# Kernel tuning notes

Measured on AMD Instinct MI355X. Metric: run time of the kernel, lower is better.

Reference implementation:

```python
import jax, jax.numpy as jnp
import numpy as np
import math

B, S, D, H = 4, 2048, 512, 8
DK = D // H
EPS = 1e-6

def _xavier(key, shape):
    fan_in, fan_out = shape[1], shape[0]
    a = math.sqrt(6.0 / (fan_in + fan_out))
    return jax.random.uniform(key, shape, jnp.float32, -a, a)

def setup_inputs() -> dict:
    key = jax.random.key(0)
    ks = jax.random.split(key, 8)
    return {
        "x_q": jax.random.normal(ks[0], (B, S, D), jnp.float32),
        "x_k": jax.random.normal(ks[1], (B, S, D), jnp.float32),
        "Wq": _xavier(ks[2], (D, D)),
        "Wk": _xavier(ks[3], (D, D)),
        "Wv": _xavier(ks[4], (D, D)),
        "Wg": jnp.zeros((D, D), jnp.float32),      # gating weight init to 0
        "bg": jnp.ones((D,), jnp.float32),          # gating bias init to 1
        "Wo": _xavier(ks[5], (D, D)),
        "bo": jnp.zeros((D,), jnp.float32),
        "gamma": jnp.ones((D,), jnp.float32),
        "beta": jnp.zeros((D,), jnp.float32),
    }

def _ln(x, gamma, beta):
    mu = jnp.mean(x, axis=-1, keepdims=True)
    var = jnp.var(x, axis=-1, keepdims=True)
    return (x - mu) * jax.lax.rsqrt(var + EPS) * gamma + beta

def reference(x_q, x_k, Wq, Wk, Wv, Wg, bg, Wo, bo, gamma, beta):
    xq = _ln(x_q, gamma, beta)          # [B,S,D]
    xk = _ln(x_k, gamma, beta)
    q = xq @ Wq.T                        # nn.Linear: x @ W^T (no bias)
    k = xk @ Wk.T
    v = xk @ Wv.T
    q = q.reshape(B, S, H, DK)
    k = k.reshape(B, S, H, DK)
    v = v.reshape(B, S, H, DK)
    attn = jnp.einsum('bshd,bthd->bhst', q, k) / math.sqrt(DK)  # [B,H,S,S]
    attn = jax.nn.softmax(attn, axis=-1) * jax.nn.softmax(attn, axis=-2)
    out = jnp.einsum('bhst,bthd->bshd', attn, v).reshape(B, S, D)
    gate = jax.nn.sigmoid(xq @ Wg.T + bg)
    return (out * gate) @ Wo.T + bo
```

## Files before the change

kernel.cpp:

```cpp
#include <hip/hip_runtime.h>

#define BB 4
#define SS 2048
#define DD 512
#define HH 8
#define RR (BB * SS)
#define BH (BB * HH)

typedef unsigned short u16;
typedef unsigned int   u32;
typedef __attribute__((ext_vector_type(4))) float f32x4;
typedef __attribute__((ext_vector_type(8))) short bf16x8;

__device__ __forceinline__ float bf2f(u16 u) { return __uint_as_float(((u32)u) << 16); }
__device__ __forceinline__ u16 f2bf(float f) {
    u32 x = __float_as_uint(f);
    return (u16)((x + 0x7fffu + ((x >> 16) & 1u)) >> 16);
}
__device__ __forceinline__ bool is_bf16(const void* gamma) {
    return *(const u32*)gamma == 0x3F803F80u;
}
__device__ __forceinline__ float ldin(const void* p, size_t i, bool b16) {
    return b16 ? bf2f(((const u16*)p)[i]) : ((const float*)p)[i];
}
__device__ __forceinline__ float expc(float x) { return __expf(fminf(x, 60.f)); }
__device__ __forceinline__ float e2sum(float x) {
    return __builtin_amdgcn_exp2f(fminf(x * 1.44269504f, 86.5617f));
}
__device__ __forceinline__ float e2pv(float x) {
    return __builtin_amdgcn_exp2f(fminf(x * 2.88539008f, 86.5617f));
}

__global__ __launch_bounds__(256) void k_ln(
    const void* xq, const void* xk, const void* gamma, const void* beta,
    u16* __restrict__ lnq, u16* __restrict__ lnk, float* l_col)
{
    bool b16 = is_bf16(gamma);
    int row = blockIdx.x, tid = threadIdx.x;
    const void* x = blockIdx.y ? xk : xq;
    u16* o = blockIdx.y ? lnk : lnq;
    size_t base = (size_t)row * DD;

    if (blockIdx.y == 0 && row < 256) l_col[row * 256 + tid] = 0.f;

    float x0 = ldin(x, base + tid * 2, b16);
    float x1 = ldin(x, base + tid * 2 + 1, b16);
    float s = x0 + x1, ss = x0 * x0 + x1 * x1;
    for (int m = 1; m < 64; m <<= 1) { s += __shfl_xor(s, m); ss += __shfl_xor(ss, m); }
    __shared__ float ws4[4], wss4[4], mu_s, rs_s;
    int wv = tid >> 6;
    if ((tid & 63) == 0) { ws4[wv] = s; wss4[wv] = ss; }
    __syncthreads();
    if (tid == 0) {
        float S1 = ws4[0] + ws4[1] + ws4[2] + ws4[3];
        float S2 = wss4[0] + wss4[1] + wss4[2] + wss4[3];
        float mu = S1 / (float)DD;
        float var = S2 / (float)DD - mu * mu;
        mu_s = mu; rs_s = rsqrtf(fmaxf(var, 0.f) + 1e-6f);
    }
    __syncthreads();
    float mu = mu_s, rstd = rs_s;
    float g0 = ldin(gamma, tid * 2, b16), g1 = ldin(gamma, tid * 2 + 1, b16);
    float b0 = ldin(beta, tid * 2, b16),  b1 = ldin(beta, tid * 2 + 1, b16);
    o[base + tid * 2]     = f2bf((x0 - mu) * rstd * g0 + b0);
    o[base + tid * 2 + 1] = f2bf((x1 - mu) * rstd * g1 + b1);
}

__global__ __launch_bounds__(256) void k_proj4(
    const u16* __restrict__ lnq, const u16* __restrict__ lnk,
    const void* Wq, const void* Wk, const void* Wv, const void* Wg,
    const void* bg, const void* gamma,
    u16* __restrict__ qb, u16* __restrict__ kb,
    u16* __restrict__ vT, u16* __restrict__ gb)
{
    __shared__ __align__(16) u16 As[128][64];
    __shared__ __align__(16) u16 Bs[128][64];
    bool b16 = is_bf16(gamma);
    int which = blockIdx.z;
    const u16* A = (which <= 1) ? lnq : lnk;
    const void* W = (which == 0) ? Wq : (which == 1) ? Wg : (which == 2) ? Wk : Wv;
    u16* C = (which == 0) ? qb : (which == 1) ? gb : (which == 2) ? kb : vT;

    int tid = threadIdx.x;
    int lane = tid & 63, wave = tid >> 6;
    int r = lane & 15, q4 = lane >> 4;
    int m0 = blockIdx.y * 128, n0 = blockIdx.x * 128;
    int moff = (wave >> 1) * 64, noff = (wave & 1) * 64;
    const int K = DD, N = DD;

    f32x4 acc[4][4];
    for (int i = 0; i < 4; ++i)
        for (int j = 0; j < 4; ++j) acc[i][j] = (f32x4){0.f, 0.f, 0.f, 0.f};

    for (int k0 = 0; k0 < K; k0 += 64) {
        #pragma unroll
        for (int t = 0; t < 4; ++t) {
            int e = t * 2048 + tid * 8;
            int row = e >> 6, kk = e & 63;
            int ksw = kk ^ ((row & 7) * 8);
            *(uint4*)&As[row][ksw] = *(const uint4*)&A[(size_t)(m0 + row) * K + k0 + kk];
            if (b16) {
                *(uint4*)&Bs[row][ksw] =
                    *(const uint4*)&((const u16*)W)[(size_t)(n0 + row) * K + k0 + kk];
            } else {
                const float* wp = (const float*)W + (size_t)(n0 + row) * K + k0 + kk;
                float4 w0 = *(const float4*)wp;
                float4 w1 = *(const float4*)(wp + 4);
                ushort4 lo, hi;
                lo.x = f2bf(w0.x); lo.y = f2bf(w0.y); lo.z = f2bf(w0.z); lo.w = f2bf(w0.w);
                hi.x = f2bf(w1.x); hi.y = f2bf(w1.y); hi.z = f2bf(w1.z); hi.w = f2bf(w1.w);
                *(ushort4*)&Bs[row][ksw] = lo;
                *(ushort4*)&Bs[row][ksw + 4] = hi;
            }
        }
        __syncthreads();
        #pragma unroll
        for (int ksp = 0; ksp < 2; ++ksp) {
            int kb2 = ksp * 32 + q4 * 8;
            bf16x8 af[4], bfr[4];
            #pragma unroll
            for (int i = 0; i < 4; ++i) {
                int rowm = moff + i * 16 + r;
                af[i] = *(const bf16x8*)&As[rowm][kb2 ^ ((rowm & 7) * 8)];
                int rown = noff + i * 16 + r;
                bfr[i] = *(const bf16x8*)&Bs[rown][kb2 ^ ((rown & 7) * 8)];
            }
            #pragma unroll
            for (int i = 0; i < 4; ++i)
                #pragma unroll
                for (int j = 0; j < 4; ++j)
                    acc[i][j] = __builtin_amdgcn_mfma_f32_16x16x32_bf16(af[i], bfr[j], acc[i][j], 0, 0, 0);
        }
        __syncthreads();
    }

    if (which == 3) {
        int b = m0 >> 11;
        int sb = (m0 & 2047) + moff + q4 * 4;
        #pragma unroll
        for (int j = 0; j < 4; ++j) {
            int n = n0 + noff + j * 16 + r;
            int h = n >> 6, dkl = n & 63;
            size_t vbase = (((size_t)b * 8 + h) * 64 + dkl) * SS;
            #pragma unroll
            for (int i = 0; i < 4; ++i) {
                ushort4 wv;
                wv.x = f2bf(acc[i][j][0]); wv.y = f2bf(acc[i][j][1]);
                wv.z = f2bf(acc[i][j][2]); wv.w = f2bf(acc[i][j][3]);
                *(ushort4*)&C[vbase + sb + i * 16] = wv;
            }
        }
    } else {
        #pragma unroll
        for (int j = 0; j < 4; ++j) {
            int col = n0 + noff + j * 16 + r;
            float bj = (which == 1) ? ldin(bg, col, b16) : 0.f;
            #pragma unroll
            for (int i = 0; i < 4; ++i) {
                int rowb = m0 + moff + i * 16 + q4 * 4;
                #pragma unroll
                for (int g = 0; g < 4; ++g) {
                    float v = acc[i][j][g];
                    if (which == 1) v = 1.f / (1.f + expc(-(v + bj)));
                    else if (which == 0) v *= 0.125f;
                    C[(size_t)(rowb + g) * N + col] = f2bf(v);
                }
            }
        }
    }
}

__global__ __launch_bounds__(256) void k_sum(
    const u16* __restrict__ qm, const u16* __restrict__ km,
    float* __restrict__ l_row, float* __restrict__ l_col)
{
    __shared__ __align__(16) u16 Qs[64][64];
    __shared__ __align__(16) u16 Ks[128][64];
    __shared__ float colS[SS];
    int tid = threadIdx.x, lane = tid & 63, wave = tid >> 6;
    int r = lane & 15, q4 = lane >> 4;
    int s0 = blockIdx.x * 64;
    int bh = blockIdx.y, b = bh >> 3, h = bh & 7;
    size_t hb = (size_t)b * SS * DD + (size_t)h * 64;

    #pragma unroll
    for (int t = 0; t < 2; ++t) {
        int e = t * 2048 + tid * 8;
        int row = e >> 6, kk = e & 63;
        *(uint4*)&Qs[row][kk ^ ((row & 7) * 8)] = *(const uint4*)&qm[hb + (size_t)(s0 + row) * DD + kk];
    }
    for (int i = tid; i < SS; i += 256) colS[i] = 0.f;
    __syncthreads();

    int moff = wave * 16;
    bf16x8 aq[2];
    #pragma unroll
    for (int ksp = 0; ksp < 2; ++ksp) {
        int rowm = moff + r;
        aq[ksp] = *(const bf16x8*)&Qs[rowm][(ksp * 32 + q4 * 8) ^ ((rowm & 7) * 8)];
    }

    float rs[4] = {};
    for (int t0 = 0; t0 < SS; t0 += 128) {
        #pragma unroll
        for (int t = 0; t < 4; ++t) {
            int e = t * 2048 + tid * 8;
            int row = e >> 6, kk = e & 63;
            *(uint4*)&Ks[row][kk ^ ((row & 7) * 8)] = *(const uint4*)&km[hb + (size_t)(t0 + row) * DD + kk];
        }
        __syncthreads();

        f32x4 acc[8];
        for (int j = 0; j < 8; ++j) acc[j] = (f32x4){0.f, 0.f, 0.f, 0.f};
        #pragma unroll
        for (int ksp = 0; ksp < 2; ++ksp) {
            int kb2 = ksp * 32 + q4 * 8;
            bf16x8 bk[8];
            #pragma unroll
            for (int j = 0; j < 8; ++j) {
                int n = j * 16 + r;
                bk[j] = *(const bf16x8*)&Ks[n][kb2 ^ ((n & 7) * 8)];
            }
            #pragma unroll
            for (int j = 0; j < 8; ++j)
                acc[j] = __builtin_amdgcn_mfma_f32_16x16x32_bf16(aq[ksp], bk[j], acc[j], 0, 0, 0);
        }

        #pragma unroll
        for (int j = 0; j < 8; ++j) {
            float e0 = e2sum(acc[j][0]);
            float e1 = e2sum(acc[j][1]);
            float e2 = e2sum(acc[j][2]);
            float e3 = e2sum(acc[j][3]);
            rs[0] += e0; rs[1] += e1; rs[2] += e2; rs[3] += e3;
            float v = (e0 + e1) + (e2 + e3);
            v += __shfl_xor(v, 16); v += __shfl_xor(v, 32);
            if (q4 == 0) atomicAdd(&colS[t0 + j * 16 + r], v);
        }
        __syncthreads();
    }
    #pragma unroll
    for (int g = 0; g < 4; ++g) {
        float v = rs[g];
        v += __shfl_xor(v, 1); v += __shfl_xor(v, 2);
        v += __shfl_xor(v, 4); v += __shfl_xor(v, 8);
        if (r == 0) l_row[(size_t)bh * SS + s0 + moff + q4 * 4 + g] = v;
    }
    for (int i = tid; i < SS; i += 256)
        atomicAdd(&l_col[(size_t)bh * SS + i], colS[i]);
}

__global__ void k_rcp(const float* __restrict__ l_row, float* __restrict__ inv_r, int n)
{
    int i = blockIdx.x * blockDim.x + threadIdx.x;
    if (i < n) inv_r[i] = 1.f / fmaxf(l_row[i], 1e-30f);
}

__global__ __launch_bounds__(256) void k_vscale(
    u16* __restrict__ vT, const float* __restrict__ l_col)
{
    int row = blockIdx.x;
    int bh = row >> 6;
    int t = threadIdx.x * 8;
    size_t base = (size_t)row * SS + t;
    const float* lc = &l_col[(size_t)bh * SS + t];
    bf16x8 v = *(const bf16x8*)&vT[base];
    float4 c0 = *(const float4*)lc;
    float4 c1 = *(const float4*)(lc + 4);
    float s[8] = {1.f / fmaxf(c0.x, 1e-30f), 1.f / fmaxf(c0.y, 1e-30f),
                  1.f / fmaxf(c0.z, 1e-30f), 1.f / fmaxf(c0.w, 1e-30f),
                  1.f / fmaxf(c1.x, 1e-30f), 1.f / fmaxf(c1.y, 1e-30f),
                  1.f / fmaxf(c1.z, 1e-30f), 1.f / fmaxf(c1.w, 1e-30f)};
    bf16x8 o;
    #pragma unroll
    for (int e = 0; e < 8; ++e)
        o[e] = (short)f2bf(bf2f((u16)v[e]) * s[e]);
    *(bf16x8*)&vT[base] = o;
}

__global__ __launch_bounds__(256) void k_pv(
    const u16* __restrict__ qm, const u16* __restrict__ km, const u16* __restrict__ vT,
    const float* __restrict__ inv_r,
    const u16* __restrict__ gate, u16* __restrict__ og)
{
    __shared__ __align__(16) u16 Ep[64][128];
    __shared__ __align__(16) u16 KV[8192];
    int tid = threadIdx.x, lane = tid & 63, wave = tid >> 6;
    int r = lane & 15, q4 = lane >> 4;
    int s0 = blockIdx.x * 64;
    int bh = blockIdx.y, b = bh >> 3, h = bh & 7;
    size_t hb = (size_t)b * SS * DD + (size_t)h * 64;
    int moff = wave * 16;

    #pragma unroll
    for (int t = 0; t < 2; ++t) {
        int e = t * 2048 + tid * 8;
        int row = e >> 6, kk = e & 63;
        *(uint4*)&Ep[row][kk ^ ((row & 7) * 8)] = *(const uint4*)&qm[hb + (size_t)(s0 + row) * DD + kk];
    }
    __syncthreads();
    bf16x8 aq[2];
    #pragma unroll
    for (int ksp = 0; ksp < 2; ++ksp) {
        int rowm = moff + r;
        aq[ksp] = *(const bf16x8*)&Ep[rowm][(ksp * 32 + q4 * 8) ^ ((rowm & 7) * 8)];
    }
    __syncthreads();

    f32x4 acco[4];
    for (int j = 0; j < 4; ++j) acco[j] = (f32x4){0.f, 0.f, 0.f, 0.f};

    int sl = moff + r, swz = (sl & 7) * 8;

    for (int t0 = 0; t0 < SS; t0 += 128) {
        #pragma unroll
        for (int t = 0; t < 4; ++t) {
            int e = t * 2048 + tid * 8;
            int row = e >> 6, kk = e & 63;
            *(uint4*)&KV[row * 64 + (kk ^ ((row & 7) * 8))] =
                *(const uint4*)&km[hb + (size_t)(t0 + row) * DD + kk];
        }
        __syncthreads();

        f32x4 accs[8];
        #pragma unroll
        for (int m = 0; m < 8; ++m) accs[m] = (f32x4){0.f, 0.f, 0.f, 0.f};
        #pragma unroll
        for (int ksp = 0; ksp < 2; ++ksp) {
            int kb2 = ksp * 32 + q4 * 8;
            bf16x8 ak[8];
            #pragma unroll
            for (int m = 0; m < 8; ++m) {
                int n = m * 16 + r;
                ak[m] = *(const bf16x8*)&KV[n * 64 + (kb2 ^ ((n & 7) * 8))];
            }
            #pragma unroll
            for (int m = 0; m < 8; ++m)
                accs[m] = __builtin_amdgcn_mfma_f32_16x16x32_bf16(ak[m], aq[ksp], accs[m], 0, 0, 0);
        }
        __syncthreads();

        #pragma unroll
        for (int c = 0; c < 4; ++c) {
            int e = c * 256 + tid;
            int row = e >> 4, tc = (e & 15) * 8;
            *(uint4*)&KV[row * 128 + (tc ^ ((row & 7) * 8))] =
                *(const uint4*)&vT[((size_t)bh * 64 + row) * SS + t0 + tc];
        }
        #pragma unroll
        for (int m = 0; m < 8; ++m) {
            float p0 = e2pv(accs[m][0]);
            float p1 = e2pv(accs[m][1]);
            float p2 = e2pv(accs[m][2]);
            float p3 = e2pv(accs[m][3]);
            u32 w0, w1;
            asm("v_cvt_pk_bf16_f32 %0, %1, %2" : "=v"(w0) : "v"(p0), "v"(p1));
            asm("v_cvt_pk_bf16_f32 %0, %1, %2" : "=v"(w1) : "v"(p2), "v"(p3));
            uint2 pr; pr.x = w0; pr.y = w1;
            *(uint2*)&Ep[sl][(m * 16 + q4 * 4) ^ swz] = pr;
        }
        __syncthreads();

        #pragma unroll
        for (int ksp = 0; ksp < 4; ++ksp) {
            int kb2 = ksp * 32 + q4 * 8;
            bf16x8 ap = *(const bf16x8*)&Ep[sl][kb2 ^ swz];
            bf16x8 bv[4];
            #pragma unroll
            for (int j = 0; j < 4; ++j) {
                int n = j * 16 + r;
                bv[j] = *(const bf16x8*)&KV[n * 128 + (kb2 ^ ((n & 7) * 8))];
            }
            #pragma unroll
            for (int j = 0; j < 4; ++j)
                acco[j] = __builtin_amdgcn_mfma_f32_16x16x32_bf16(ap, bv[j], acco[j], 0, 0, 0);
        }
        __syncthreads();
    }

    #pragma unroll
    for (int g = 0; g < 4; ++g) {
        int srow = s0 + moff + q4 * 4 + g;
        float ir = inv_r[(size_t)bh * SS + srow];
        size_t ob = (size_t)b * SS * DD + (size_t)srow * DD + (size_t)h * 64;
        #pragma unroll
        for (int j = 0; j < 4; ++j) {
            int dk = j * 16 + r;
            og[ob + dk] = f2bf(acco[j][g] * ir * bf2f(gate[ob + dk]));
        }
    }
}

__global__ __launch_bounds__(256) void k_gemm_out(
    const u16* __restrict__ A, const void* W, const void* gamma,
    float* __restrict__ Cf, const void* bias)
{
    __shared__ __align__(16) u16 As[128][64];
    __shared__ __align__(16) u16 Bs[128][64];
    bool b16 = is_bf16(gamma);
    int tid = threadIdx.x;
    int lane = tid & 63, wave = tid >> 6;
    int r = lane & 15, q4 = lane >> 4;
    int m0 = blockIdx.y * 128, n0 = blockIdx.x * 128;
    int moff = (wave >> 1) * 64, noff = (wave & 1) * 64;
    const int K = DD, N = DD;

    f32x4 acc[4][4];
    for (int i = 0; i < 4; ++i)
        for (int j = 0; j < 4; ++j) acc[i][j] = (f32x4){0.f, 0.f, 0.f, 0.f};

    for (int k0 = 0; k0 < K; k0 += 64) {
        #pragma unroll
        for (int t = 0; t < 4; ++t) {
            int e = t * 2048 + tid * 8;
            int row = e >> 6, kk = e & 63;
            int ksw = kk ^ ((row & 7) * 8);
            *(uint4*)&As[row][ksw] = *(const uint4*)&A[(size_t)(m0 + row) * K + k0 + kk];
            if (b16) {
                *(uint4*)&Bs[row][ksw] =
                    *(const uint4*)&((const u16*)W)[(size_t)(n0 + row) * K + k0 + kk];
            } else {
                const float* wp = (const float*)W + (size_t)(n0 + row) * K + k0 + kk;
                float4 w0 = *(const float4*)wp;
                float4 w1 = *(const float4*)(wp + 4);
                ushort4 lo, hi;
                lo.x = f2bf(w0.x); lo.y = f2bf(w0.y); lo.z = f2bf(w0.z); lo.w = f2bf(w0.w);
                hi.x = f2bf(w1.x); hi.y = f2bf(w1.y); hi.z = f2bf(w1.z); hi.w = f2bf(w1.w);
                *(ushort4*)&Bs[row][ksw] = lo;
                *(ushort4*)&Bs[row][ksw + 4] = hi;
            }
        }
        __syncthreads();
        #pragma unroll
        for (int ksp = 0; ksp < 2; ++ksp) {
            int kb2 = ksp * 32 + q4 * 8;
            bf16x8 af[4], bfr[4];
            #pragma unroll
            for (int i = 0; i < 4; ++i) {
                int rowm = moff + i * 16 + r;
                af[i] = *(const bf16x8*)&As[rowm][kb2 ^ ((rowm & 7) * 8)];
                int rown = noff + i * 16 + r;
                bfr[i] = *(const bf16x8*)&Bs[rown][kb2 ^ ((rown & 7) * 8)];
            }
            #pragma unroll
            for (int i = 0; i < 4; ++i)
                #pragma unroll
                for (int j = 0; j < 4; ++j)
                    acc[i][j] = __builtin_amdgcn_mfma_f32_16x16x32_bf16(af[i], bfr[j], acc[i][j], 0, 0, 0);
        }
        __syncthreads();
    }
    #pragma unroll
    for (int j = 0; j < 4; ++j) {
        int col = n0 + noff + j * 16 + r;
        float bj = ldin(bias, col, b16);
        #pragma unroll
        for (int i = 0; i < 4; ++i) {
            int rowb = m0 + moff + i * 16 + q4 * 4;
            #pragma unroll
            for (int g = 0; g < 4; ++g) {
                float v = acc[i][j][g] + bj;
                size_t idx = (size_t)(rowb + g) * N + col;
                if (b16) ((u16*)Cf)[idx] = f2bf(v);
                else     Cf[idx] = v;
            }
        }
    }
}

extern "C" void kernel_launch(void* const* d_in, const int* in_sizes, int n_in,
                              void* d_out, int out_size, void* d_ws, size_t ws_size,
                              hipStream_t stream)
{
    const void* x_q   = d_in[0];
    const void* x_k   = d_in[1];
    const void* Wq    = d_in[2];
    const void* Wk    = d_in[3];
    const void* Wv    = d_in[4];
    const void* Wg    = d_in[5];
    const void* bg    = d_in[6];
    const void* Wo    = d_in[7];
    const void* bo    = d_in[8];
    const void* gamma = d_in[9];
    const void* beta  = d_in[10];

    char* base = (char*)d_ws;
    u16* lnq = (u16*)(base);
    u16* lnk = (u16*)(base + (size_t) 8 * 1024 * 1024);
    u16* qb  = (u16*)(base + (size_t)16 * 1024 * 1024);
    u16* kb  = (u16*)(base + (size_t)24 * 1024 * 1024);
    u16* gb  = (u16*)(base + (size_t)32 * 1024 * 1024);
    float* l_row = (float*)(base + (size_t)40 * 1024 * 1024);
    float* l_col = (float*)(base + (size_t)40 * 1024 * 1024 + 262144);
    float* inv_r = (float*)(base + (size_t)40 * 1024 * 1024 + 524288);
    u16* vT = (u16*)d_out;
    u16* og = lnk;

    k_ln<<<dim3(RR, 2), 256, 0, stream>>>(x_q, x_k, gamma, beta, lnq, lnk, l_col);

    k_proj4<<<dim3(4, 64, 4), 256, 0, stream>>>(lnq, lnk, Wq, Wk, Wv, Wg, bg, gamma,
                                                qb, kb, vT, gb);

    k_sum<<<dim3(SS / 64, BH), 256, 0, stream>>>(qb, kb, l_row, l_col);
    k_rcp<<<dim3(BH * SS / 256), 256, 0, stream>>>(l_row, inv_r, BH * SS);
    k_vscale<<<dim3(BH * 64), 256, 0, stream>>>(vT, l_col);
    k_pv<<<dim3(SS / 64, BH), 256, 0, stream>>>(qb, kb, vT, inv_r, gb, og);

    k_gemm_out<<<dim3(4, 64), 256, 0, stream>>>(og, Wo, gamma, (float*)d_out, bo);
}
```

Baseline: 334.0 us.

## Double-buffer K tiles in k_sum with register prefetch

Restructures the k_sum loop to double-buffer K tiles in shared memory and prefetch the tile after next into registers. Global load latency can then overlap with the MFMA and exp-sum work on the current tile. This costs an extra 16KB of LDS and more registers, which may lower occupancy.

```diff
diff --git a/kernel.cpp b/kernel.cpp
--- a/kernel.cpp
+++ b/kernel.cpp
@@ -175,7 +175,7 @@
     float* __restrict__ l_row, float* __restrict__ l_col)
 {
     __shared__ __align__(16) u16 Qs[64][64];
-    __shared__ __align__(16) u16 Ks[128][64];
+    __shared__ __align__(16) u16 Ks[2][128][64];
     __shared__ float colS[SS];
     int tid = threadIdx.x, lane = tid & 63, wave = tid >> 6;
     int r = lane & 15, q4 = lane >> 4;
@@ -183,13 +183,21 @@
     int bh = blockIdx.y, b = bh >> 3, h = bh & 7;
     size_t hb = (size_t)b * SS * DD + (size_t)h * 64;
 
+    int se = tid * 8;
+    int srow = se >> 6, skk = se & 63;
+    int ssw = skk ^ ((srow & 7) * 8);
+
     #pragma unroll
     for (int t = 0; t < 2; ++t) {
-        int e = t * 2048 + tid * 8;
+        int e = t * 2048 + se;
         int row = e >> 6, kk = e & 63;
         *(uint4*)&Qs[row][kk ^ ((row & 7) * 8)] = *(const uint4*)&qm[hb + (size_t)(s0 + row) * DD + kk];
     }
     for (int i = tid; i < SS; i += 256) colS[i] = 0.f;
+    uint4 kreg[4];
+    #pragma unroll
+    for (int t = 0; t < 4; ++t)
+        kreg[t] = *(const uint4*)&km[hb + (size_t)(t * 32 + srow) * DD + skk];
     __syncthreads();
 
     int moff = wave * 16;
@@ -199,18 +207,30 @@
         int rowm = moff + r;
         aq[ksp] = *(const bf16x8*)&Qs[rowm][(ksp * 32 + q4 * 8) ^ ((rowm & 7) * 8)];
     }
+    #pragma unroll
+    for (int t = 0; t < 4; ++t)
+        *(uint4*)&Ks[0][t * 32 + srow][ssw] = kreg[t];
+    #pragma unroll
+    for (int t = 0; t < 4; ++t)
+        kreg[t] = *(const uint4*)&km[hb + (size_t)(128 + t * 32 + srow) * DD + skk];
+    __syncthreads();
 
     float rs[4] = {};
-    for (int t0 = 0; t0 < SS; t0 += 128) {
-        #pragma unroll
-        for (int t = 0; t < 4; ++t) {
-            int e = t * 2048 + tid * 8;
-            int row = e >> 6, kk = e & 63;
-            *(uint4*)&Ks[row][kk ^ ((row & 7) * 8)] = *(const uint4*)&km[hb + (size_t)(t0 + row) * DD + kk];
-        }
-        __syncthreads();
-
+    for (int it = 0; it < 16; ++it) {
+        int cur = it & 1, t0 = it * 128;
+        if (it < 15) {
+            #pragma unroll
+            for (int t = 0; t < 4; ++t)
+                *(uint4*)&Ks[cur ^ 1][t * 32 + srow][ssw] = kreg[t];
+            if (it < 14) {
+                int tn = t0 + 256;
+                #pragma unroll
+                for (int t = 0; t < 4; ++t)
+                    kreg[t] = *(const uint4*)&km[hb + (size_t)(tn + t * 32 + srow) * DD + skk];
+            }
+        }
         f32x4 acc[8];
+        #pragma unroll
         for (int j = 0; j < 8; ++j) acc[j] = (f32x4){0.f, 0.f, 0.f, 0.f};
         #pragma unroll
         for (int ksp = 0; ksp < 2; ++ksp) {
@@ -219,13 +239,12 @@
             #pragma unroll
             for (int j = 0; j < 8; ++j) {
                 int n = j * 16 + r;
-                bk[j] = *(const bf16x8*)&Ks[n][kb2 ^ ((n & 7) * 8)];
+                bk[j] = *(const bf16x8*)&Ks[cur][n][kb2 ^ ((n & 7) * 8)];
             }
             #pragma unroll
             for (int j = 0; j < 8; ++j)
                 acc[j] = __builtin_amdgcn_mfma_f32_16x16x32_bf16(aq[ksp], bk[j], acc[j], 0, 0, 0);
         }
-
         #pragma unroll
         for (int j = 0; j < 8; ++j) {
             float e0 = e2sum(acc[j][0]);
```

New measurement: 374.2 us. 1.12x slower.
